# Performance work log

Measured on AMD Instinct MI355X. Metric: run time of the kernel, lower is better.

## Reference

```python
import math
import jax, jax.numpy as jnp
import numpy as np

K_KDE = 50
K_RIPS = 16
SCALE = 30.0
DESTNUM = 10
THRESHOLD = 1.0  # hardcoded in topograd_loss
N, D = 8192, 64


def _knn(x, k):
    """Brute-force k-NN with squared L2 distances (faiss IndexFlatL2 semantics,
    self included as nearest neighbour). Returns (sq_dists[N,k], idxs[N,k]),
    neighbours sorted by increasing distance."""
    sq = jnp.sum(x * x, axis=1)
    d = sq[:, None] + sq[None, :] - 2.0 * (x @ x.T)  # [N,N]
    neg, idx = jax.lax.top_k(-d, k)
    return -neg, idx


def _cluster(density, rips_idxs, threshold):
    """Union-find re-implementation of the numba `cluster` routine.
    Iterates points from high density (index N-1) to low; each point joins the
    entry of its highest-index upward neighbour; other upward neighbours'
    entries are merged if their persistence is below threshold, and every
    cross-entry comparison emits a persistence pair (entry_idx, ref_idx).
    Returns the raw pers_pairs array (without the [-1,-1] sentinel rows)."""
    n = density.shape[0]
    parent = np.arange(n)
    name = np.arange(n)  # name[root] = entry id (a point index)

    def find(i):
        root = i
        while parent[root] != root:
            root = parent[root]
        while parent[i] != root:  # path compression
            parent[i], i = root, parent[i]
        return root

    pairs = []
    for i in range(n - 2, -1, -1):
        nbr = rips_idxs[i]
        us = nbr[nbr > i]  # upward (denser, already-processed) neighbours
        if us.size == 0:
            continue  # point i forms its own singleton entry
        e_up = name[find(int(us.max()))]
        parent[find(i)] = find(e_up)  # append i to entry e_up
        for j in us:
            ei = name[find(int(j))]
            if ei != e_up:
                pairs.append((ei, i))
                if density[ei] - density[i] < threshold:
                    parent[find(ei)] = find(e_up)  # merge entry ei into e_up
    return np.asarray(pairs, dtype=np.int64).reshape(-1, 2)


def _pd_pairs(pairs, n):
    """For each unique entry id in pairs[:,0], keep (entry_id, max ref idx)."""
    maxref = np.full(n, -1, dtype=np.int64)
    np.maximum.at(maxref, pairs[:, 0], pairs[:, 1])
    uniq = np.unique(pairs[:, 0])
    return np.stack([uniq, maxref[uniq]], axis=1)


def setup_inputs() -> dict:
    key = jax.random.key(0)
    x = jax.random.normal(key, (N, D), dtype=jnp.float32)
    return {"x": x}


def reference(x):
    # --- KNN kernel density estimate (differentiable) ---
    vals, _ = _knn(x, K_KDE)
    res = jnp.sum(jnp.exp(-vals / SCALE), axis=1) / (K_KDE * SCALE)
    dens = res / jnp.max(res)
    # --- sort by ascending density ---
    sorted_idxs = jnp.argsort(dens)
    dens_s = dens[sorted_idxs]
    x_s = x[sorted_idxs]
    # --- delta-Rips graph on sorted points ---
    _, rips_idxs = _knn(x_s, K_RIPS)
    # --- persistence clustering (non-differentiable, host) ---
    pairs = _cluster(np.asarray(dens_s), np.asarray(rips_idxs), THRESHOLD)
    pd = jnp.asarray(_pd_pairs(pairs, x.shape[0]))  # [P,2] int64
    # --- topological loss ---
    oripd = dens_s[pd]  # [P,2] (birth, death) densities
    sidx = jnp.argsort(oripd[:, 0] - oripd[:, 1])  # ascending persistence
    changepairs = pd[sidx[:-DESTNUM]]
    nochangepairs = pd[sidx[-DESTNUM:-1]]
    dest = jax.lax.stop_gradient(oripd[sidx[-1]])  # torch.as_tensor detaches
    pd11 = dens_s[changepairs]
    weakdist = jnp.sum(pd11[:, 0] - pd11[:, 1]) / math.sqrt(2.0)
    strongdist = jnp.sum(jnp.linalg.norm(dens_s[nochangepairs] - dest, axis=1))
    return weakdist + strongdist
```

## Files before the change

kernel.cpp:

```cpp
#include <hip/hip_runtime.h>
#include <stdint.h>

#define NN 8192
#define DD 64

using bf16x8 = __attribute__((ext_vector_type(8))) short;
using f32x4  = __attribute__((ext_vector_type(4))) float;

__device__ __forceinline__ unsigned short f2bf(float f){
  unsigned u = __float_as_uint(f);
  return (unsigned short)((u + 0x7FFFu + ((u >> 16) & 1u)) >> 16);
}

__device__ __forceinline__ unsigned long long shfl64_xor(unsigned long long v, int off){
  return (((unsigned long long)(unsigned)__shfl_xor((int)(v >> 32), off)) << 32)
       | (unsigned long long)(unsigned)__shfl_xor((int)(v & 0xFFFFFFFFu), off);
}

__global__ __launch_bounds__(256) void k_pre(const float* __restrict__ x, float* __restrict__ xT,
                                             float* __restrict__ sq, int do_tr,
                                             uint4* __restrict__ xfrag, int do_frag){
  __shared__ float tile[64*65];
  const int tid = threadIdx.x;
  const int b = blockIdx.x;
  for (int k = 0; k < 4; ++k){
    const int idx4 = tid + k*256;
    const float4 v = ((const float4*)(x + (size_t)b*4096))[idx4];
    const int row = idx4 >> 4, d0 = (idx4 & 15) * 4;
    tile[row*65 + d0 + 0] = v.x;
    tile[row*65 + d0 + 1] = v.y;
    tile[row*65 + d0 + 2] = v.z;
    tile[row*65 + d0 + 3] = v.w;
  }
  __syncthreads();
  if (do_tr){
    const int jj = tid & 15;
    const int dq = tid >> 4;
    for (int k = 0; k < 4; ++k){
      const int d = dq + 16*k;
      float4 o;
      o.x = tile[(jj*4+0)*65 + d];
      o.y = tile[(jj*4+1)*65 + d];
      o.z = tile[(jj*4+2)*65 + d];
      o.w = tile[(jj*4+3)*65 + d];
      ((float4*)xT)[(size_t)d*2048 + b*16 + jj] = o;
    }
  }
  if (do_frag){
    for (int ch = tid; ch < 512; ch += 256){
      const int c  = ch & 15;
      const int q  = (ch >> 4) & 3;
      const int m  = (ch >> 6) & 1;
      const int gl = ch >> 7;
      const float* sp = tile + (gl*16 + c)*65 + m*32 + q*8;
      unsigned short h[8];
#pragma unroll
      for (int i2 = 0; i2 < 8; ++i2) h[i2] = f2bf(sp[i2]);
      uint4 o;
      o.x = (unsigned)h[0] | ((unsigned)h[1] << 16);
      o.y = (unsigned)h[2] | ((unsigned)h[3] << 16);
      o.z = (unsigned)h[4] | ((unsigned)h[5] << 16);
      o.w = (unsigned)h[6] | ((unsigned)h[7] << 16);
      xfrag[(size_t)b*512 + ch] = o;
    }
  }
  if (tid < 64){
    float acc = 0.f;
    const float* rp = tile + tid*65;
    for (int d = 0; d < 64; ++d) acc = fmaf(rp[d], rp[d], acc);
    sq[b*64 + tid] = acc;
  }
}

template<bool XT>
__device__ __forceinline__ void dists_1024(const float* __restrict__ x, const float* __restrict__ xT,
                                           const float* __restrict__ xi, int jbase, int tid,
                                           float acc[8][4]){
#pragma unroll
  for (int r = 0; r < 8; ++r)
#pragma unroll
    for (int q = 0; q < 4; ++q) acc[r][q] = 0.f;
  const int j0 = jbase + tid*4;
  for (int dq = 0; dq < 16; ++dq){
    float4 vj[4];
    if (XT){
#pragma unroll
      for (int s = 0; s < 4; ++s)
        vj[s] = ((const float4*)xT)[(size_t)(dq*4+s)*2048 + (j0 >> 2)];
    } else {
#pragma unroll
      for (int s = 0; s < 4; ++s){
        const int d = dq*4 + s;
        vj[s].x = x[(size_t)(j0+0)*64 + d];
        vj[s].y = x[(size_t)(j0+1)*64 + d];
        vj[s].z = x[(size_t)(j0+2)*64 + d];
        vj[s].w = x[(size_t)(j0+3)*64 + d];
      }
    }
#pragma unroll
    for (int r = 0; r < 8; ++r){
      const float4 wv = ((const float4*)(xi + r*64))[dq];
      acc[r][0] = fmaf(vj[0].x, wv.x, acc[r][0]);
      acc[r][1] = fmaf(vj[0].y, wv.x, acc[r][1]);
      acc[r][2] = fmaf(vj[0].z, wv.x, acc[r][2]);
      acc[r][3] = fmaf(vj[0].w, wv.x, acc[r][3]);
      acc[r][0] = fmaf(vj[1].x, wv.y, acc[r][0]);
      acc[r][1] = fmaf(vj[1].y, wv.y, acc[r][1]);
      acc[r][2] = fmaf(vj[1].z, wv.y, acc[r][2]);
      acc[r][3] = fmaf(vj[1].w, wv.y, acc[r][3]);
      acc[r][0] = fmaf(vj[2].x, wv.z, acc[r][0]);
      acc[r][1] = fmaf(vj[2].y, wv.z, acc[r][1]);
      acc[r][2] = fmaf(vj[2].z, wv.z, acc[r][2]);
      acc[r][3] = fmaf(vj[2].w, wv.z, acc[r][3]);
      acc[r][0] = fmaf(vj[3].x, wv.w, acc[r][0]);
      acc[r][1] = fmaf(vj[3].y, wv.w, acc[r][1]);
      acc[r][2] = fmaf(vj[3].z, wv.w, acc[r][2]);
      acc[r][3] = fmaf(vj[3].w, wv.w, acc[r][3]);
    }
  }
}

template<bool XT>
__global__ __launch_bounds__(256) void k_samp(const float* __restrict__ x, const float* __restrict__ xT,
                                              const float* __restrict__ sq, float* __restrict__ tub){
  __shared__ __align__(16) float xi[8*64];
  __shared__ float sqi_s[8];
  __shared__ __align__(16) float samp[8*1024];
  const int tid = threadIdx.x;
  const int i0 = blockIdx.x * 8;
  for (int t = tid; t < 8*64; t += 256) xi[t] = x[(size_t)i0*64 + t];
  if (tid < 8) sqi_s[tid] = sq[i0+tid];
  __syncthreads();
  float sqir[8];
#pragma unroll
  for (int r = 0; r < 8; ++r) sqir[r] = sqi_s[r];

  const int w0 = (blockIdx.x * 1024) & 8191;
  float acc[8][4];
  dists_1024<XT>(x, xT, xi, w0, tid, acc);
  float sqj[4];
#pragma unroll
  for (int q = 0; q < 4; ++q) sqj[q] = sq[w0 + tid*4 + q];
#pragma unroll
  for (int r = 0; r < 8; ++r)
#pragma unroll
    for (int q = 0; q < 4; ++q)
      samp[r*1024 + tid*4 + q] = (sqir[r] + sqj[q]) - 2.f*acc[r][q];
  __syncthreads();
  const int wv = tid >> 6, lane = tid & 63;
  for (int rr = 0; rr < 2; ++rr){
    const int r = wv + rr*4;
    float v[16];
#pragma unroll
    for (int k2 = 0; k2 < 16; ++k2) v[k2] = samp[r*1024 + lane + 64*k2];
    unsigned lo = 0u, hi = 0x7F800001u;
    while (hi - lo > 1u){
      const unsigned mid = (lo + hi) >> 1;
      const float pf = __uint_as_float(mid);
      int c = 0;
#pragma unroll
      for (int k2 = 0; k2 < 16; ++k2) c += (v[k2] < pf) ? 1 : 0;
#pragma unroll
      for (int off = 32; off; off >>= 1) c += __shfl_xor(c, off);
      if (c >= 32) hi = mid; else lo = mid;
    }
    if (lane == 0) tub[i0 + r] = __uint_as_float(hi);
  }
}

__global__ __launch_bounds__(256) void k_filt(const float* __restrict__ x, const float* __restrict__ sq,
                                              const float* __restrict__ tub,
                                              const uint4* __restrict__ xfrag,
                                              unsigned char* __restrict__ nib){
  const int tid = threadIdx.x;
  const int l   = tid & 63;
  const int w   = tid >> 6;
  const int qh  = l >> 4;
  const int c16 = l & 15;
  const int i0  = blockIdx.x * 8;

  bf16x8 a0, a1;
#pragma unroll
  for (int i2 = 0; i2 < 8; ++i2){ a0[i2] = 0; a1[i2] = 0; }
  if (c16 < 8){
    const float* ap = x + (size_t)(i0 + c16)*64 + qh*8;
#pragma unroll
    for (int i2 = 0; i2 < 8; ++i2){
      a0[i2] = (short)f2bf(ap[i2]);
      a1[i2] = (short)f2bf(ap[i2 + 32]);
    }
  }
  float thr3[4], rs[4];
#pragma unroll
  for (int rg = 0; rg < 4; ++rg){
    int row = qh*4 + rg; row = (row < 8) ? row : 0;
    thr3[rg] = (tub[i0 + row] - sq[i0 + row]) + 0.002f;
    rs[rg]   = 0.017f * sqrtf(sq[i0 + row]);
  }

  const bf16x8* bfp = (const bf16x8*)xfrag + (size_t)w*128 + l;
  const float*  sqp = sq + w*16 + c16;
  unsigned char* nb = nib + (size_t)blockIdx.x*8192 + w*16 + c16;

  bf16x8 A0 = bfp[0],   A1 = bfp[64];     float SA = sqp[0];
  bf16x8 B0 = bfp[512], B1 = bfp[512+64]; float SB = sqp[64];
  for (int it = 0; it < 128; it += 2){
    const int n2 = (it+2 < 128) ? it+2 : 126;
    const int n3 = (it+3 < 128) ? it+3 : 127;
    bf16x8 N0 = bfp[(size_t)n2*512], N1 = bfp[(size_t)n2*512 + 64];
    bf16x8 M0 = bfp[(size_t)n3*512], M1 = bfp[(size_t)n3*512 + 64];
    const float SN = sqp[n2*64], SM = sqp[n3*64];
    {
      f32x4 acc = {0.f, 0.f, 0.f, 0.f};
      acc = __builtin_amdgcn_mfma_f32_16x16x32_bf16(a0, A0, acc, 0, 0, 0);
      acc = __builtin_amdgcn_mfma_f32_16x16x32_bf16(a1, A1, acc, 0, 0, 0);
      const float sr = sqrtf(SA);
      unsigned m4 = 0u;
      m4 |= (fmaf(-rs[0], sr, fmaf(-2.f, acc[0], SA)) < thr3[0]) ? 1u : 0u;
      m4 |= (fmaf(-rs[1], sr, fmaf(-2.f, acc[1], SA)) < thr3[1]) ? 2u : 0u;
      m4 |= (fmaf(-rs[2], sr, fmaf(-2.f, acc[2], SA)) < thr3[2]) ? 4u : 0u;
      m4 |= (fmaf(-rs[3], sr, fmaf(-2.f, acc[3], SA)) < thr3[3]) ? 8u : 0u;
      const unsigned pm = (unsigned)__shfl((int)m4, (l + 16) & 63);
      if (l < 16) nb[it*64] = (unsigned char)(m4 | (pm << 4));
    }
    {
      f32x4 acc = {0.f, 0.f, 0.f, 0.f};
      acc = __builtin_amdgcn_mfma_f32_16x16x32_bf16(a0, B0, acc, 0, 0, 0);
      acc = __builtin_amdgcn_mfma_f32_16x16x32_bf16(a1, B1, acc, 0, 0, 0);
      const float sr = sqrtf(SB);
      unsigned m4 = 0u;
      m4 |= (fmaf(-rs[0], sr, fmaf(-2.f, acc[0], SB)) < thr3[0]) ? 1u : 0u;
      m4 |= (fmaf(-rs[1], sr, fmaf(-2.f, acc[1], SB)) < thr3[1]) ? 2u : 0u;
      m4 |= (fmaf(-rs[2], sr, fmaf(-2.f, acc[2], SB)) < thr3[2]) ? 4u : 0u;
      m4 |= (fmaf(-rs[3], sr, fmaf(-2.f, acc[3], SB)) < thr3[3]) ? 8u : 0u;
      const unsigned pm = (unsigned)__shfl((int)m4, (l + 16) & 63);
      if (l < 16) nb[(it+1)*64] = (unsigned char)(m4 | (pm << 4));
    }
    A0 = N0; A1 = N1; SA = SN;
    B0 = M0; B1 = M1; SB = SM;
  }
}

__global__ __launch_bounds__(256, 8) void k_csort(const float* __restrict__ x, const float* __restrict__ sq,
                                                  const float* __restrict__ tub,
                                                  const unsigned char* __restrict__ nib,
                                                  float* __restrict__ res, unsigned short* __restrict__ nn16){
  __shared__ __align__(16) float xi[4*68];
  __shared__ float sqi_s[4];
  __shared__ float tubs[4];
  __shared__ __align__(16) unsigned long long cand[4*512];
  __shared__ unsigned ccnt[4];
  const int tid  = threadIdx.x;
  const int grp  = blockIdx.x >> 1;
  const int half = blockIdx.x & 1;
  const int i0   = grp*8 + half*4;
  const unsigned rmask = half ? 0xF0F0F0F0u : 0x0F0F0F0Fu;

  for (int t = tid; t < 4*64; t += 256) xi[(t >> 6)*68 + (t & 63)] = x[(size_t)i0*64 + t];
  if (tid < 4){ sqi_s[tid] = sq[i0+tid]; tubs[tid] = tub[i0+tid]; ccnt[tid] = 0u; }
  for (int t = tid; t < 4*512; t += 256) cand[t] = ~0ULL;
  __syncthreads();

  const uint4* nb4 = (const uint4*)(nib + (size_t)grp*8192);
  for (int u = tid; u < 512; u += 256){
    const uint4 v4 = nb4[u];
    unsigned wds[4] = {v4.x & rmask, v4.y & rmask, v4.z & rmask, v4.w & rmask};
#pragma unroll
    for (int ww = 0; ww < 4; ++ww){
      unsigned wvv = wds[ww];
      while (wvv){
        const int bit = __builtin_ctz(wvv);
        wvv &= wvv - 1u;
        const int r = bit & 3;
        const int j = u*16 + ww*4 + (bit >> 3);
        const float* xj = x + (size_t)j*64;
        const float* xr = xi + r*68;
        float acc = 0.f;
#pragma unroll
        for (int d4 = 0; d4 < 16; ++d4){
          const float4 vj4 = ((const float4*)xj)[d4];
          const float4 wi4 = ((const float4*)xr)[d4];
          acc = fmaf(vj4.x, wi4.x, acc);
          acc = fmaf(vj4.y, wi4.y, acc);
          acc = fmaf(vj4.z, wi4.z, acc);
          acc = fmaf(vj4.w, wi4.w, acc);
        }
        const float dist = (sqi_s[r] + sq[j]) - 2.f*acc;
        if (dist < tubs[r]){
          const unsigned pos = atomicAdd(&ccnt[r], 1u);
          if (pos < 512u){
            unsigned u2 = __float_as_uint(dist);
            u2 = ((int)u2 < 0) ? ~u2 : (u2 | 0x80000000u);
            cand[r*512 + pos] = (((unsigned long long)u2) << 13) | (unsigned)j;
          }
        }
      }
    }
  }
  __syncthreads();

  const int w = tid >> 6, lane = tid & 63;
  {
    const int r = w;
    unsigned long long k8[8];
#pragma unroll
    for (int t = 0; t < 8; ++t) k8[t] = cand[r*512 + lane + 64*t];

    const unsigned long long REALMAX = (1ULL << 45) - 1ULL;
    int creal = 0;
#pragma unroll
    for (int t = 0; t < 8; ++t) creal += (int)__popcll(__ballot(k8[t] <= REALMAX));

    unsigned long long K50;
    if (creal >= 50){
      unsigned long long lo = 0ULL, hi = REALMAX;
      while (lo < hi){
        const unsigned long long mid = lo + ((hi - lo) >> 1);
        int c = 0;
#pragma unroll
        for (int t = 0; t < 8; ++t) c += (int)__popcll(__ballot(k8[t] <= mid));
        if (c >= 50) hi = mid; else lo = mid + 1ULL;
      }
      K50 = hi;
    } else {
      K50 = ~0ULL;
    }

    unsigned long long* buf = cand + r*512;
    buf[lane] = ~0ULL;
    int base = 0;
#pragma unroll
    for (int t = 0; t < 8; ++t){
      const bool pr = (k8[t] <= K50) && (k8[t] != ~0ULL);
      const unsigned long long bal = __ballot(pr);
      const int off = base + (int)__popcll(bal & ((1ULL << lane) - 1ULL));
      if (pr && off < 64) buf[off] = k8[t];
      base += (int)__popcll(bal);
    }
    unsigned long long key = buf[lane];

#pragma unroll
    for (int k = 2; k <= 64; k <<= 1){
#pragma unroll
      for (int j = k >> 1; j > 0; j >>= 1){
        const unsigned long long p = shfl64_xor(key, j);
        const bool dirUp = ((lane & k) == 0);
        const bool lower = ((lane & j) == 0);
        const unsigned long long mn = (key < p) ? key : p;
        const unsigned long long mx = (key < p) ? p : key;
        key = (dirUp == lower) ? mn : mx;
      }
    }

    float e = 0.f;
    if (lane < 50){
      unsigned u2 = (unsigned)(key >> 13);
      u2 = (u2 & 0x80000000u) ? (u2 & 0x7FFFFFFFu) : ~u2;
      e = expf(-__uint_as_float(u2) / 30.f);
    }
#pragma unroll
    for (int off = 32; off; off >>= 1) e += __shfl_down(e, off);
    if (lane == 0) res[i0+r] = e / 1500.f;
    if (lane < 16) nn16[(size_t)(i0+r)*16 + lane] = (unsigned short)(key & 8191ULL);
  }
}

template<bool XT>
__global__ __launch_bounds__(256) void k_cand(const float* __restrict__ x, const float* __restrict__ xT,
                                              const float* __restrict__ sq,
                                              float* __restrict__ res, unsigned short* __restrict__ nn16){
  __shared__ float xi[8*64];
  __shared__ float sqi_s[8];
  __shared__ float tubs[8];
  __shared__ __align__(16) unsigned long long cand[8*512];
  __shared__ unsigned ccnt[8];
  float* samp = (float*)cand;
  const int tid = threadIdx.x;
  const int i0 = blockIdx.x * 8;
  for (int t = tid; t < 8*64; t += 256) xi[t] = x[(size_t)i0*64 + t];
  if (tid < 8){ sqi_s[tid] = sq[i0+tid]; ccnt[tid] = 0u; }
  __syncthreads();
  float sqir[8];
#pragma unroll
  for (int r = 0; r < 8; ++r) sqir[r] = sqi_s[r];

  const int w0 = (blockIdx.x * 1024) & 8191;
  {
    float acc[8][4];
    dists_1024<XT>(x, xT, xi, w0, tid, acc);
    float sqj[4];
#pragma unroll
    for (int q = 0; q < 4; ++q) sqj[q] = sq[w0 + tid*4 + q];
#pragma unroll
    for (int r = 0; r < 8; ++r)
#pragma unroll
      for (int q = 0; q < 4; ++q)
        samp[r*1024 + tid*4 + q] = (sqir[r] + sqj[q]) - 2.f*acc[r][q];
  }
  __syncthreads();
  {
    const int wv = tid >> 6, lane = tid & 63;
    for (int rr = 0; rr < 2; ++rr){
      const int r = wv + rr*4;
      float v[16];
#pragma unroll
      for (int k2 = 0; k2 < 16; ++k2) v[k2] = samp[r*1024 + lane + 64*k2];
      unsigned lo = 0u, hi = 0x7F800001u;
      while (hi - lo > 1u){
        const unsigned mid = (lo + hi) >> 1;
        const float pf = __uint_as_float(mid);
        int c = 0;
#pragma unroll
        for (int k2 = 0; k2 < 16; ++k2) c += (v[k2] < pf) ? 1 : 0;
#pragma unroll
        for (int off = 32; off; off >>= 1) c += __shfl_xor(c, off);
        if (c >= 32) hi = mid; else lo = mid;
      }
      if (lane == 0) tubs[r] = __uint_as_float(hi);
    }
  }
  __syncthreads();
  float tubr[8];
#pragma unroll
  for (int r = 0; r < 8; ++r) tubr[r] = tubs[r];
  for (int t = tid; t < 8*512; t += 256) cand[t] = ~0ULL;
  __syncthreads();

  for (int pass = 0; pass < 8; ++pass){
    const int jb = pass*1024;
    float acc[8][4];
    dists_1024<XT>(x, xT, xi, jb, tid, acc);
    const int j0 = jb + tid*4;
    float sqj[4];
#pragma unroll
    for (int q = 0; q < 4; ++q) sqj[q] = sq[j0 + q];
#pragma unroll
    for (int r = 0; r < 8; ++r){
#pragma unroll
      for (int q = 0; q < 4; ++q){
        const float dist = (sqir[r] + sqj[q]) - 2.f*acc[r][q];
        if (dist < tubr[r]){
          const unsigned pos = atomicAdd(&ccnt[r], 1u);
          if (pos < 512u){
            unsigned u = __float_as_uint(dist);
            u = ((int)u < 0) ? ~u : (u | 0x80000000u);
            cand[r*512 + pos] = (((unsigned long long)u) << 13) | (unsigned)(j0 + q);
          }
        }
      }
    }
  }
  __syncthreads();

  for (int k = 2; k <= 512; k <<= 1){
    for (int jj2 = k >> 1; jj2 > 0; jj2 >>= 1){
      const int mm = tid;
      const int i = ((mm & ~(jj2-1)) << 1) | (mm & (jj2-1));
      const int p = i | jj2;
      const bool up2 = ((i & k) == 0);
#pragma unroll
      for (int r = 0; r < 8; ++r){
        unsigned long long a = cand[r*512+i], bb = cand[r*512+p];
        if ((a > bb) == up2){ cand[r*512+i] = bb; cand[r*512+p] = a; }
      }
      __syncthreads();
    }
  }

  const int wv2 = tid >> 6, lane2 = tid & 63;
  for (int rr = 0; rr < 2; ++rr){
    const int r = wv2*2 + rr;
    const unsigned long long kk = cand[r*512 + lane2];
    float e = 0.f;
    if (lane2 < 50){
      unsigned u2 = (unsigned)(kk >> 13);
      u2 = (u2 & 0x80000000u) ? (u2 & 0x7FFFFFFFu) : ~u2;
      e = expf(-__uint_as_float(u2) / 30.f);
    }
#pragma unroll
    for (int off = 32; off; off >>= 1) e += __shfl_down(e, off);
    if (lane2 == 0) res[i0+r] = e / 1500.f;
    if (lane2 < 16) nn16[(size_t)(i0+r)*16 + lane2] = (unsigned short)(kk & 8191ULL);
  }
}

__global__ __launch_bounds__(256) void k_rank(const float* __restrict__ res,
                                              unsigned short* __restrict__ rank,
                                              float* __restrict__ dens_s){
  __shared__ __align__(16) unsigned long long keys[NN];
  __shared__ float red[256];
  __shared__ unsigned short pcnt[256];
  const int tid = threadIdx.x;
  float m = 0.f;
  for (int t = tid; t < NN; t += 256) m = fmaxf(m, res[t]);
  red[tid] = m; __syncthreads();
  for (int o = 128; o; o >>= 1){ if (tid < o) red[tid] = fmaxf(red[tid], red[tid+o]); __syncthreads(); }
  const float mr = red[0];
  __syncthreads();
  for (int t = tid; t < NN; t += 256){
    const float dnv = res[t] / mr;
    keys[t] = (((unsigned long long)__float_as_uint(dnv)) << 13) | (unsigned)t;
  }
  __syncthreads();
  const int i = blockIdx.x*128 + (tid & 127);
  const unsigned long long ki = keys[i];
  const int j0 = (tid >> 7) * (NN/2);
  int c = 0;
#pragma unroll 8
  for (int j = 0; j < NN/2; ++j) c += (keys[j0 + j] < ki) ? 1 : 0;
  pcnt[tid] = (unsigned short)c;
  __syncthreads();
  if (tid < 128){
    const int r = (int)pcnt[tid] + (int)pcnt[tid + 128];
    rank[i] = (unsigned short)r;
    dens_s[r] = __uint_as_float((unsigned)(ki >> 13));
  }
}

__global__ __launch_bounds__(256) void k_ups(const unsigned short* __restrict__ rank,
                                             const unsigned short* __restrict__ nn16,
                                             unsigned short* __restrict__ ups_t){
  __shared__ __align__(16) unsigned short rk[NN];
  const int tid = threadIdx.x;
  for (int t = tid; t < NN/8; t += 256) ((uint4*)rk)[t] = ((const uint4*)rank)[t];
  __syncthreads();
  const int o = blockIdx.x*256 + tid;
  const int p = rk[o];
  const uint4 n0 = ((const uint4*)nn16)[(size_t)o*2];
  const uint4 n1 = ((const uint4*)nn16)[(size_t)o*2 + 1];
  unsigned nw[8] = {n0.x, n0.y, n0.z, n0.w, n1.x, n1.y, n1.z, n1.w};
  unsigned short outv[16];
  int cnt = 0;
  for (int k = 0; k < 16; ++k){
    const unsigned nb = (nw[k >> 1] >> ((k & 1) * 16)) & 0xFFFFu;
    const unsigned r = rk[nb];
    if ((int)r > p){
      int q = cnt++;
      while (q > 0 && outv[q-1] < (unsigned short)r){ outv[q] = outv[q-1]; --q; }
      outv[q] = (unsigned short)r;
    }
  }
  for (int k = cnt; k < 16; ++k) outv[k] = 0;
  unsigned short* dst = ups_t + (size_t)p*16;
  uint4 a, b;
  a.x = (unsigned)outv[0] | ((unsigned)outv[1] << 16);
  a.y = (unsigned)outv[2] | ((unsigned)outv[3] << 16);
  a.z = (unsigned)outv[4] | ((unsigned)outv[5] << 16);
  a.w = (unsigned)outv[6] | ((unsigned)outv[7] << 16);
  b.x = (unsigned)outv[8] | ((unsigned)outv[9] << 16);
  b.y = (unsigned)outv[10] | ((unsigned)outv[11] << 16);
  b.z = (unsigned)outv[12] | ((unsigned)outv[13] << 16);
  b.w = (unsigned)outv[14] | ((unsigned)outv[15] << 16);
  ((uint4*)dst)[0] = a;
  ((uint4*)dst)[1] = b;
}

__device__ __forceinline__ unsigned uf_find2(volatile unsigned short* comp, unsigned x){
  unsigned r = comp[x];
  while (true){
    const unsigned g = comp[r];
    if (g == r) break;
    comp[x] = (unsigned short)g;
    x = r; r = g;
  }
  return r;
}

__global__ __launch_bounds__(1024) void k_msf(const float* __restrict__ dens_s,
                                              unsigned short* __restrict__ ups_t,
                                              unsigned long long* __restrict__ edges,
                                              int edgecap,
                                              float* __restrict__ out){
  __shared__ __align__(16) float dens[NN];
  __shared__ __align__(16) unsigned short P[NN];
  __shared__ __align__(16) unsigned short pkid[NN];
  __shared__ __align__(16) unsigned short death[NN];
  __shared__ __align__(16) unsigned short pkrank[4096];
  __shared__ __align__(16) unsigned short comp[4096];
  __shared__ __align__(16) unsigned short hook[4096];
  __shared__ __align__(16) unsigned bestv[4096];
  __shared__ __align__(16) unsigned long long msf[4096];
  __shared__ unsigned long long wred[17];
  __shared__ unsigned long long sel[10];
  __shared__ unsigned ecnt_s, ecnt2_s, mcnt_s, chg_s, flat_s, dcnt_s;
  unsigned* scan1 = (unsigned*)msf;
  float* red = (float*)msf;
  unsigned* dlist = bestv;

  const int tid = threadIdx.x;
  const int lane = tid & 63;

  for (int t = tid; t < NN/4; t += 1024)
    ((float4*)dens)[t] = ((const float4*)dens_s)[t];
  for (int t = tid; t < NN; t += 1024){
    const unsigned u0 = ups_t[(size_t)t*16];
    P[t] = (u0 == 0u) ? (unsigned short)t : (unsigned short)u0;
    death[t] = 0xFFFFu;
  }
  if (tid == 0){ ecnt_s = 0u; mcnt_s = 0u; dcnt_s = 0u; }
  __syncthreads();

  for (int rd = 0; rd < 13; ++rd){
    for (int pp = 0; pp < 8; ++pp){
      const int p = tid + pp*1024;
      const unsigned v = P[p];
      const unsigned w2 = P[v];
      if (w2 != v) P[p] = (unsigned short)w2;
    }
    __syncthreads();
  }

  {
    const int p0 = tid*8;
    int c = 0;
    for (int k = 0; k < 8; ++k) c += (P[p0+k] == (unsigned short)(p0+k)) ? 1 : 0;
    scan1[tid] = (unsigned)c; __syncthreads();
    for (int s = 1; s < 1024; s <<= 1){
      const unsigned v = scan1[tid];
      const unsigned u = (tid >= s) ? scan1[tid-s] : 0u;
      __syncthreads();
      scan1[tid] = v + u;
      __syncthreads();
    }
    int base = (int)scan1[tid] - c;
    for (int k = 0; k < 8; ++k){
      const int p = p0 + k;
      if (P[p] == (unsigned short)p){
        pkid[p] = (unsigned short)base;
        if (base < 4096) pkrank[base] = (unsigned short)p;
        ++base;
      }
    }
  }
  __syncthreads();
  int Npk = (int)scan1[1023];
  if (Npk > 4096) Npk = 4096;
  __syncthreads();

  for (int pp = 0; pp < 8; ++pp){
    const int p = tid + pp*1024;
    const uint4 a4 = ((const uint4*)ups_t)[(size_t)p*2];
    const uint4 b4 = ((const uint4*)ups_t)[(size_t)p*2 + 1];
    unsigned uu[8] = {a4.x, a4.y, a4.z, a4.w, b4.x, b4.y, b4.z, b4.w};
    unsigned edv[15];
    int nd = 0;
    const unsigned u0 = uu[0] & 0xFFFFu;
    if (u0 != 0u){
      const unsigned m0 = P[u0];
      const unsigned m0id = pkid[m0];
      for (int k = 1; k < 16; ++k){
        const unsigned uk = (uu[k >> 1] >> ((k & 1) * 16)) & 0xFFFFu;
        if (uk == 0u) break;
        const unsigned v = P[uk];
        if (v == m0) continue;
        const unsigned vid = pkid[v];
        bool dup = false;
        for (int j = 0; j < nd; ++j) dup = dup || ((edv[j] >> 16) == vid);
        if (dup) continue;
        edv[nd++] = (vid << 16) | m0id;
      }
    }
    unsigned off = (unsigned)nd;
    for (int s = 1; s < 64; s <<= 1){
      const unsigned o = (unsigned)__shfl_up((int)off, s);
      if (lane >= s) off += o;
    }
    const unsigned tot = (unsigned)__shfl((int)off, 63);
    unsigned wb = 0u;
    if (lane == 0 && tot) wb = atomicAdd(&ecnt_s, tot);
    wb = (unsigned)__shfl((int)wb, 0);
    const unsigned mybase = wb + off - (unsigned)nd;
    for (int k = 0; k < nd; ++k){
      const unsigned pos = mybase + (unsigned)k;
      if ((int)pos < edgecap)
        edges[pos] = (((unsigned long long)(unsigned)p) << 32) | (unsigned long long)edv[k];
    }
  }
  __syncthreads();
  int Ecur = ((int)ecnt_s < edgecap) ? (int)ecnt_s : edgecap;

  unsigned long long* eb_in  = edges;
  unsigned long long* eb_out = (unsigned long long*)ups_t;
  for (int t = tid; t < Npk; t += 1024) comp[t] = (unsigned short)t;
  __syncthreads();
  for (int round = 0; round < 16 && Ecur > 0; ++round){
    for (int t = tid; t < Npk; t += 1024){ bestv[t] = 0u; hook[t] = 0xFFFFu; }
    if (tid == 0){ chg_s = 0u; ecnt2_s = 0u; }
    __syncthreads();
    for (int base = 0; base < Ecur; base += 1024){
      const int e = base + tid;
      bool keep = false;
      unsigned long long ed = 0ULL;
      if (e < Ecur){
        ed = eb_in[e];
        const unsigned a = (unsigned)(ed >> 16) & 0xFFFFu;
        const unsigned b = (unsigned)ed & 0xFFFFu;
        const unsigned ra = comp[a], rb = comp[b];
        if (ra != rb){
          keep = true;
          const unsigned key = ((((unsigned)(ed >> 32)) + 1u) << 18) | (unsigned)e;
          atomicMax(&bestv[ra], key);
          atomicMax(&bestv[rb], key);
        }
      }
      const unsigned long long bal = __ballot(keep);
      const unsigned cnt = (unsigned)__popcll(bal);
      const unsigned pfx = (unsigned)__popcll(bal & ((1ULL << lane) - 1ULL));
      unsigned wb = 0u;
      if (lane == 0 && cnt) wb = atomicAdd(&ecnt2_s, cnt);
      wb = (unsigned)__shfl((int)wb, 0);
      if (keep && (wb + pfx) < 32768u) eb_out[wb + pfx] = ed;
    }
    __syncthreads();
    for (int t = tid; t < Npk; t += 1024){
      if (comp[t] == (unsigned short)t && bestv[t] != 0u){
        const unsigned long long ed = eb_in[bestv[t] & 0x3FFFFu];
        const unsigned a = (unsigned)(ed >> 16) & 0xFFFFu;
        const unsigned b = (unsigned)ed & 0xFFFFu;
        const unsigned ra = comp[a], rb = comp[b];
        hook[t] = (unsigned short)((ra == (unsigned)t) ? rb : ra);
      }
    }
    __syncthreads();
    for (int t = tid; t < Npk; t += 1024){
      const unsigned o = hook[t];
      if (o != 0xFFFFu && !(hook[o] == (unsigned short)t && (unsigned)t < o)){
        comp[t] = (unsigned short)o;
        chg_s = 1u;
        const unsigned long long ed = eb_in[bestv[t] & 0x3FFFFu];
        const unsigned pos = atomicAdd(&mcnt_s, 1u);
        if (pos < 4096u) msf[pos] = (((ed >> 32) + 1ULL) << 32) | (ed & 0xFFFFFFFFULL);
      }
    }
    __syncthreads();
    for (;;){
      if (tid == 0) flat_s = 0u;
      __syncthreads();
      for (int t = tid; t < Npk; t += 1024){
        const unsigned c = comp[t];
        const unsigned cc = comp[c];
        if (cc != c){ comp[t] = (unsigned short)cc; flat_s = 1u; }
      }
      __syncthreads();
      if (flat_s == 0u) break;
    }
    const int En = ((int)ecnt2_s < 32768) ? (int)ecnt2_s : 32767;
    const unsigned ch = chg_s;
    __syncthreads();
    Ecur = En;
    { unsigned long long* t2 = eb_in; eb_in = eb_out; eb_out = t2; }
    if (ch == 0u) break;
  }

  const int M = ((int)mcnt_s < 4096) ? (int)mcnt_s : 4095;
  int W = 64; while (W < M) W <<= 1;
  for (int t = M + tid; t < W; t += 1024) msf[t] = 0ULL;
  for (int t = tid; t < Npk; t += 1024) comp[t] = (unsigned short)t;
  __syncthreads();
  for (int k = 2; k <= W; k <<= 1){
    for (int j = k >> 1; j > 0; j >>= 1){
      for (int m2 = tid; m2 < W/2; m2 += 1024){
        const int i = ((m2 & ~(j-1)) << 1) | (m2 & (j-1));
        const int p = i | j;
        const bool up = ((i & k) == 0);
        const unsigned long long a = msf[i], b = msf[p];
        if ((a < b) == up){ msf[i] = b; msf[p] = a; }
      }
      __syncthreads();
    }
  }

  {
    const int nb = (M + 63) >> 6;
    for (int bch = 0; bch < nb; ++bch){
      if (tid < 64){
        const int ei = bch*64 + lane;
        unsigned ra = 0xFFFFu, rb = 0xFFFFu, wgt = 0u;
        if (ei < M){
          const unsigned long long e = msf[ei];
          const unsigned a = ((unsigned)e >> 16) & 0xFFFFu;
          const unsigned b = (unsigned)e & 0xFFFFu;
          wgt = (unsigned)(e >> 32) - 1u;
          ra = uf_find2(comp, a);
          rb = uf_find2(comp, b);
        }
        unsigned kra = 0xFFFFu, krb = 0xFFFFu;
        for (int i = 0; i < 64; ++i){
          const unsigned rai = (unsigned)__builtin_amdgcn_readlane((int)ra, i);
          const unsigned rbi = (unsigned)__builtin_amdgcn_readlane((int)rb, i);
          if (rai == 0xFFFFu || rai == rbi) continue;
          if (lane == i){ kra = rai; krb = rbi; }
          ra = (ra == rai) ? rbi : ra;
          rb = (rb == rai) ? rbi : rb;
        }
        if (kra != 0xFFFFu){
          death[pkrank[kra]] = (unsigned short)wgt;
          comp[kra] = (unsigned short)krb;
        }
      }
      __syncthreads();
      for (int t = tid; t < Npk; t += 1024){
        const unsigned c = comp[t];
        const unsigned cc = comp[c];
        if (cc != c) comp[t] = (unsigned short)cc;
      }
      __syncthreads();
    }
  }
  __syncthreads();

  float s = 0.f;
  for (int e = tid; e < NN; e += 1024){
    const int dr = death[e];
    if (dr != 0xFFFF) s += dens[e] - dens[dr];
  }
  red[tid] = s; __syncthreads();
  for (int o = 512; o; o >>= 1){ if (tid < o) red[tid] += red[tid+o]; __syncthreads(); }
  const float S = red[0];

  for (int e8 = 0; e8 < 8; ++e8){
    const int e = tid + e8*1024;
    const int dr = death[e];
    const bool have = (dr != 0xFFFF);
    const unsigned long long bal = __ballot(have);
    const unsigned cnt = (unsigned)__popcll(bal);
    const unsigned pfx = (unsigned)__popcll(bal & ((1ULL << lane) - 1ULL));
    unsigned wb = 0u;
    if (lane == 0 && cnt) wb = atomicAdd(&dcnt_s, cnt);
    wb = (unsigned)__shfl((int)wb, 0);
    if (have && (wb + pfx) < 4096u) dlist[wb + pfx] = ((unsigned)e << 13) | (unsigned)dr;
  }
  __syncthreads();
  const int Dm = ((int)dcnt_s < 4096) ? (int)dcnt_s : 4096;

  unsigned long long last = ~0ULL;
  for (int t10 = 0; t10 < 10; ++t10){
    unsigned long long km = 0ULL;
    for (int i = tid; i < Dm; i += 1024){
      const unsigned pk = dlist[i];
      const unsigned e = pk >> 13, dr = pk & 8191u;
      const float pers = dens[e] - dens[dr];
      const unsigned long long k = (((unsigned long long)__float_as_uint(pers)) << 13) | e;
      if (k < last && k > km) km = k;
    }
    for (int off = 32; off; off >>= 1){
      const unsigned long long o = shfl64_xor(km, off);
      km = (o > km) ? o : km;
    }
    if (lane == 0) wred[tid >> 6] = km;
    __syncthreads();
    if (tid < 64){
      unsigned long long v = (tid < 16) ? wred[tid] : 0ULL;
      for (int off = 8; off; off >>= 1){
        const unsigned long long o = shfl64_xor(v, off);
        v = (o > v) ? o : v;
      }
      if (tid == 0) wred[16] = v;
    }
    __syncthreads();
    const unsigned long long st = wred[16];
    if (tid == 0) sel[t10] = st;
    last = st;
    __syncthreads();
  }
  if (tid == 0){
    float top = 0.f;
    for (int t10 = 0; t10 < 10; ++t10)
      if (sel[t10]) top += __uint_as_float((unsigned)(sel[t10] >> 13));
    float strong = 0.f, dest0 = 0.f, dest1 = 0.f;
    if (sel[0]){
      const unsigned e0 = (unsigned)(sel[0] & 8191ULL);
      dest0 = dens[e0]; dest1 = dens[death[e0]];
    }
    for (int t10 = 1; t10 < 10; ++t10){
      if (!sel[t10]) continue;
      const unsigned e = (unsigned)(sel[t10] & 8191ULL);
      const float a = dens[e] - dest0;
      const float b = dens[death[e]] - dest1;
      strong += sqrtf(a*a + b*b);
    }
    out[0] = (S - top) / 1.41421356237309515f + strong;
  }
}

extern "C" void kernel_launch(void* const* d_in, const int* in_sizes, int n_in,
                              void* d_out, int out_size, void* d_ws, size_t ws_size,
                              hipStream_t stream){
  const float* x = (const float*)d_in[0];
  char* w = (char*)d_ws;
  float*          sq     = (float*)(w + 0);
  float*          res    = (float*)(w + 32768);
  float*          dens_s = (float*)(w + 65536);
  unsigned short* rank   = (unsigned short*)(w + 98304);
  unsigned short* nn16   = (unsigned short*)(w + 114688);
  unsigned short* ups_t  = (unsigned short*)(w + 376832);
  float*          xT     = (float*)(w + 655360);
  uint4*          xfrag  = (uint4*)(w + 2752512);
  float*          tub    = (float*)(w + 3801088);
  unsigned char*  nib    = (unsigned char*)(w + 3833856);
  const int use_xt  = (ws_size >= (size_t)2752512) ? 1 : 0;
  const int use_mf2 = (ws_size >= (size_t)(3833856 + 8*1024*1024)) ? 1 : 0;
  unsigned long long* edges = use_xt ? (unsigned long long*)(w + 655360)
                                     : (unsigned long long*)(w + 114688);
  const int edgecap = use_xt ? 262143 : 32767;

  k_pre<<<128, 256, 0, stream>>>(x, xT, sq, use_xt, xfrag, use_mf2);
  if (use_mf2){
    k_samp<true><<<1024, 256, 0, stream>>>(x, xT, sq, tub);
    k_filt<<<1024, 256, 0, stream>>>(x, sq, tub, xfrag, nib);
    k_csort<<<2048, 256, 0, stream>>>(x, sq, tub, nib, res, nn16);
  } else if (use_xt){
    k_cand<true ><<<1024, 256, 0, stream>>>(x, xT, sq, res, nn16);
  } else {
    k_cand<false><<<1024, 256, 0, stream>>>(x, xT, sq, res, nn16);
  }
  k_rank<<<64, 256, 0, stream>>>(res, rank, dens_s);
  k_ups <<<32, 256, 0, stream>>>(rank, nn16, ups_t);
  k_msf <<<1, 1024, 0, stream>>>(dens_s, ups_t, edges, edgecap, (float*)d_out);
}
```

Measured before the change: 570.8 us.

## Cut block-wide barriers in k_msf scan, Kruskal batches and top-10 selection

Replaces the Hillis-Steele shared-memory prefix scan over 1024 threads with a wavefront shuffle scan plus a small cross-wave scan. The Kruskal batch loop now runs entirely inside a single wavefront and drops the per-batch barriers and the full-block comp pointer-jumping pass, relying on uf_find2 path handling alone. The top-10 persistence selection also runs in one wavefront, removing two barriers per iteration. This trades idle-thread parallelism for far fewer __syncthreads, but union-find finds may get longer without the compression pass.

```diff
diff --git a/kernel.cpp b/kernel.cpp
--- a/kernel.cpp
+++ b/kernel.cpp
@@ -580,7 +580,6 @@
   __shared__ __align__(16) unsigned short hook[4096];
   __shared__ __align__(16) unsigned bestv[4096];
   __shared__ __align__(16) unsigned long long msf[4096];
-  __shared__ unsigned long long wred[17];
   __shared__ unsigned long long sel[10];
   __shared__ unsigned ecnt_s, ecnt2_s, mcnt_s, chg_s, flat_s, dcnt_s;
   unsigned* scan1 = (unsigned*)msf;
@@ -614,15 +613,26 @@
     const int p0 = tid*8;
     int c = 0;
     for (int k = 0; k < 8; ++k) c += (P[p0+k] == (unsigned short)(p0+k)) ? 1 : 0;
-    scan1[tid] = (unsigned)c; __syncthreads();
-    for (int s = 1; s < 1024; s <<= 1){
-      const unsigned v = scan1[tid];
-      const unsigned u = (tid >= s) ? scan1[tid-s] : 0u;
-      __syncthreads();
-      scan1[tid] = v + u;
-      __syncthreads();
-    }
-    int base = (int)scan1[tid] - c;
+    unsigned v = (unsigned)c;
+    for (int s = 1; s < 64; s <<= 1){
+      const unsigned o = (unsigned)__shfl_up((int)v, s);
+      if (lane >= s) v += o;
+    }
+    if (lane == 63) scan1[1024 + (tid >> 6)] = v;
+    __syncthreads();
+    if (tid < 16){
+      unsigned wv2 = scan1[1024 + tid];
+      for (int s = 1; s < 16; s <<= 1){
+        const unsigned o = (unsigned)__shfl_up((int)wv2, s);
+        if (tid >= s) wv2 += o;
+      }
+      scan1[1040 + tid] = wv2;
+    }
+    __syncthreads();
+    const unsigned woff = (tid >= 64) ? scan1[1040 + (tid >> 6) - 1] : 0u;
+    const unsigned incl = v + woff;
+    if (tid == 1023) scan1[1023] = incl;
+    int base = (int)incl - c;
     for (int k = 0; k < 8; ++k){
       const int p = p0 + k;
       if (P[p] == (unsigned short)p){
@@ -772,8 +782,8 @@
 
   {
     const int nb = (M + 63) >> 6;
-    for (int bch = 0; bch < nb; ++bch){
-      if (tid < 64){
+    if (tid < 64){
+      for (int bch = 0; bch < nb; ++bch){
         const int ei = bch*64 + lane;
         unsigned ra = 0xFFFFu, rb = 0xFFFFu, wgt = 0u;
         if (ei < M){
@@ -798,16 +808,9 @@
           comp[kra] = (unsigned short)krb;
         }
       }
-      __syncthreads();
-      for (int t = tid; t < Npk; t += 1024){
-        const unsigned c = comp[t];
-        const unsigned cc = comp[c];
-        if (cc != c) comp[t] = (unsigned short)cc;
-      }
-      __syncthreads();
-    }
-  }
-  __syncthreads();
+    }
+    __syncthreads();
+  }
 
   float s = 0.f;
   for (int e = tid; e < NN; e += 1024){
@@ -833,36 +836,26 @@
   __syncthreads();
   const int Dm = ((int)dcnt_s < 4096) ? (int)dcnt_s : 4096;
 
-  unsigned long long last = ~0ULL;
-  for (int t10 = 0; t10 < 10; ++t10){
-    unsigned long long km = 0ULL;
-    for (int i = tid; i < Dm; i += 1024){
-      const unsigned pk = dlist[i];
-      const unsigned e = pk >> 13, dr = pk & 8191u;
-      const float pers = dens[e] - dens[dr];
-      const unsigned long long k = (((unsigned long long)__float_as_uint(pers)) << 13) | e;
-      if (k < last && k > km) km = k;
-    }
-    for (int off = 32; off; off >>= 1){
-      const unsigned long long o = shfl64_xor(km, off);
-      km = (o > km) ? o : km;
-    }
-    if (lane == 0) wred[tid >> 6] = km;
-    __syncthreads();
-    if (tid < 64){
-      unsigned long long v = (tid < 16) ? wred[tid] : 0ULL;
-      for (int off = 8; off; off >>= 1){
-        const unsigned long long o = shfl64_xor(v, off);
-        v = (o > v) ? o : v;
-      }
-      if (tid == 0) wred[16] = v;
-    }
-    __syncthreads();
-    const unsigned long long st = wred[16];
-    if (tid == 0) sel[t10] = st;
-    last = st;
-    __syncthreads();
-  }
+  if (tid < 64){
+    unsigned long long last = ~0ULL;
+    for (int t10 = 0; t10 < 10; ++t10){
+      unsigned long long km = 0ULL;
+      for (int i = lane; i < Dm; i += 64){
+        const unsigned pk = dlist[i];
+        const unsigned e = pk >> 13, dr = pk & 8191u;
+        const float pers = dens[e] - dens[dr];
+        const unsigned long long k = (((unsigned long long)__float_as_uint(pers)) << 13) | e;
+        if (k < last && k > km) km = k;
+      }
+      for (int off = 32; off; off >>= 1){
+        const unsigned long long o = shfl64_xor(km, off);
+        km = (o > km) ? o : km;
+      }
+      if (lane == 0) sel[t10] = km;
+      last = km;
+    }
+  }
+  __syncthreads();
   if (tid == 0){
     float top = 0.f;
     for (int t10 = 0; t10 < 10; ++t10)
```

Measured after the change: 561.6 us. Within noise of the previous version (-1.6%).
